# Optimization experiments

Hardware: AMD Instinct MI355X
Metric: run time of the kernel (lower is better)

The kernel has to match this reference:

```python
import jax, jax.numpy as jnp
import numpy as np

N_NODES = 100000
N_EDGES = 1200000
N_FEAT = 128
HIDDEN = 64
N_CLASSES = 40


def setup_inputs() -> dict:
    key = jax.random.key(0)
    k1, k2, k3, k4 = jax.random.split(key, 4)
    x = jax.random.normal(k1, (N_NODES, N_FEAT), dtype=jnp.float32)
    edge_index = jax.random.randint(k2, (2, N_EDGES), 0, N_NODES, dtype=jnp.int64)
    # Glorot-style init for the linear weights (as in PyG GCNConv)
    W1 = jax.random.normal(k3, (N_FEAT, HIDDEN), dtype=jnp.float32) * (1.0 / np.sqrt(N_FEAT))
    b1 = jnp.zeros((HIDDEN,), dtype=jnp.float32)
    W2 = jax.random.normal(k4, (HIDDEN, N_CLASSES), dtype=jnp.float32) * (1.0 / np.sqrt(HIDDEN))
    b2 = jnp.zeros((N_CLASSES,), dtype=jnp.float32)
    return {"x": x, "edge_index": edge_index, "W1": W1, "b1": b1, "W2": W2, "b2": b2}


def _gcn_conv(x, row, col, dinv, W, b):
    # x: [N, Fin], W: [Fin, Fout]. Transform then normalized scatter-add aggregation.
    h = x @ W                                  # [N, Fout]
    norm = dinv[row] * dinv[col]               # [E'] symmetric normalization
    msgs = h[row] * norm[:, None]              # [E', Fout] gather + scale
    out = jax.ops.segment_sum(msgs, col, num_segments=x.shape[0])  # scatter-add
    return out + b


def reference(x, edge_index, W1, b1, W2, b2):
    N = x.shape[0]
    loops = jnp.arange(N, dtype=edge_index.dtype)
    # add self loops (PyG GCNConv default)
    row = jnp.concatenate([edge_index[0], loops])
    col = jnp.concatenate([edge_index[1], loops])
    deg = jax.ops.segment_sum(jnp.ones_like(col, dtype=x.dtype), col, num_segments=N)
    dinv = jax.lax.rsqrt(deg)  # deg >= 1 thanks to self loops
    h = jax.nn.relu(_gcn_conv(x, row, col, dinv, W1, b1))
    # dropout is identity at inference (training=False)
    return _gcn_conv(h, row, col, dinv, W2, b2)
```

## Files before the change

### kernel.cpp

```cpp
#include <hip/hip_runtime.h>
#include <hip/hip_fp16.h>
#include <type_traits>

#define N_NODES 100000
#define N_EDGES 1200000
#define N_FEAT 128
#define HIDDEN 64
#define N_CLASSES 40

#define BSHIFT 9
#define BMASK 511
#define BUCKET_NODES 512
#define NBK ((N_NODES + BUCKET_NODES - 1) / BUCKET_NODES)
#define BCAP 8192
#define CHUNK 2048

typedef _Float16 f16x8 __attribute__((ext_vector_type(8)));
typedef float f32x4 __attribute__((ext_vector_type(4)));


__global__ __launch_bounds__(256) void bucket_kernel(const int* __restrict__ row,
                                                     const int* __restrict__ col,
                                                     int* __restrict__ gcursor,
                                                     unsigned* __restrict__ bke, int E) {
    __shared__ int hist[NBK];
    __shared__ int pfx[NBK];
    __shared__ int gbase[NBK];
    __shared__ int lcnt[NBK];
    __shared__ unsigned ord[CHUNK];
    __shared__ unsigned char obkt[CHUNK];

    const int t = threadIdx.x;
    const int e0 = blockIdx.x * CHUNK;
    const int nE = min(CHUNK, E - e0);

    for (int i = t; i < NBK; i += 256) {
        hist[i] = 0;
        lcnt[i] = 0;
    }
    __syncthreads();

    for (int i = t; i < nE; i += 256) atomicAdd(&hist[col[e0 + i] >> BSHIFT], 1);
    __syncthreads();

    int v = (t < NBK) ? hist[t] : 0;
    if (t < NBK) pfx[t] = v;
    __syncthreads();
    for (int d = 1; d < 256; d <<= 1) {
        int add = (t >= d && t < NBK) ? pfx[t - d] : 0;
        __syncthreads();
        if (t < NBK) pfx[t] += add;
        __syncthreads();
    }
    if (t < NBK) {
        pfx[t] -= v;
        gbase[t] = t * BCAP + ((v > 0) ? atomicAdd(&gcursor[t], v) : 0);
    }
    __syncthreads();

    for (int i = t; i < nE; i += 256) {
        int r = row[e0 + i];
        int c = col[e0 + i];
        int b = c >> BSHIFT;
        int pos = pfx[b] + atomicAdd(&lcnt[b], 1);
        ord[pos] = ((unsigned)r << BSHIFT) | (unsigned)(c & BMASK);
        obkt[pos] = (unsigned char)b;
    }
    __syncthreads();

    for (int i = t; i < nE; i += 256) {
        int b = obkt[i];
        bke[(size_t)gbase[b] + (i - pfx[b])] = ord[i];
    }
}


__global__ __launch_bounds__(256) void place_kernel(const int* __restrict__ gcursor,
                                                    const unsigned* __restrict__ bke,
                                                    int* __restrict__ rowptr,
                                                    float* __restrict__ dinv,
                                                    int* __restrict__ csr_src, int n) {
    __shared__ int hist[BUCKET_NODES];
    __shared__ int cur[BUCKET_NODES];
    __shared__ int tsum[256];

    const int b = blockIdx.x, t = threadIdx.x;
    const int node0 = b << BSHIFT;
    const int nNodes = min(BUCKET_NODES, n - node0);

    const int myCnt = (t < NBK) ? gcursor[t] : 0;
    tsum[t] = myCnt;
    __syncthreads();
    for (int d = 1; d < 256; d <<= 1) {
        int add = (t >= d) ? tsum[t - d] : 0;
        __syncthreads();
        tsum[t] += add;
        __syncthreads();
    }
    const int base = tsum[b] - gcursor[b];
    const int nb = gcursor[b];
    __syncthreads();

    hist[t] = 0;
    hist[t + 256] = 0;
    __syncthreads();

    const unsigned* src = bke + (size_t)b * BCAP;
    for (int i = t; i < nb; i += 256) atomicAdd(&hist[src[i] & BMASK], 1);
    __syncthreads();

    const int c0 = hist[2 * t];
    const int c1 = hist[2 * t + 1];
    const int s = c0 + c1;
    tsum[t] = s;
    __syncthreads();
    for (int d = 1; d < 256; d <<= 1) {
        int add = (t >= d) ? tsum[t - d] : 0;
        __syncthreads();
        tsum[t] += add;
        __syncthreads();
    }
    const int e0 = base + tsum[t] - s;
    const int e1 = e0 + c0;

    cur[2 * t] = e0;
    cur[2 * t + 1] = e1;
    if (2 * t < nNodes) {
        rowptr[node0 + 2 * t] = e0;
        dinv[node0 + 2 * t] = rsqrtf((float)(c0 + 1));
    }
    if (2 * t + 1 < nNodes) {
        rowptr[node0 + 2 * t + 1] = e1;
        dinv[node0 + 2 * t + 1] = rsqrtf((float)(c1 + 1));
    }
    if (t == 0 && node0 + nNodes == n) rowptr[n] = N_EDGES;
    __syncthreads();

    for (int i = t; i < nb; i += 256) {
        unsigned p = src[i];
        int pos = atomicAdd(&cur[p & BMASK], 1);
        csr_src[pos] = (int)(p >> BSHIFT);
    }
}


template <typename XT, int K, int XSTRIDE, int NOUT, int NOUT_PAD, int OSTRIDE>
__global__ __launch_bounds__(256) void gemm_mfma_kernel(const XT* __restrict__ X,
                                                        const float* __restrict__ W,
                                                        const float* __restrict__ dinv,
                                                        __half* __restrict__ Hs, int M) {
    constexpr int KCH = K / 32;
    constexpr int NT = NOUT_PAD / 16;
    constexpr int WPITCH = NOUT_PAD + 2;

    __shared__ _Float16 wh[K * WPITCH];
    __shared__ float sdinv[256];

    const int tid = threadIdx.x;
    const int bnode0 = blockIdx.x * 256;

    for (int i = tid; i < K * NOUT_PAD; i += 256) {
        int k = i / NOUT_PAD, n = i % NOUT_PAD;
        wh[k * WPITCH + n] = (n < NOUT) ? (_Float16)W[k * NOUT + n] : (_Float16)0.0f;
    }
    {
        int node = bnode0 + tid;
        sdinv[tid] = (node < M) ? dinv[node] : 0.f;
    }
    __syncthreads();

    const int wid = tid >> 6;
    const int lane = tid & 63;
    const int m = lane & 15;
    const int quad = lane >> 4;

    f16x8 bf[KCH][NT];
#pragma unroll
    for (int kc = 0; kc < KCH; ++kc)
#pragma unroll
        for (int nt = 0; nt < NT; ++nt)
#pragma unroll
            for (int j = 0; j < 8; ++j)
                bf[kc][nt][j] = wh[(kc * 32 + quad * 8 + j) * WPITCH + nt * 16 + m];

    for (int nt4 = 0; nt4 < 4; ++nt4) {
        const int nb = bnode0 + wid * 64 + nt4 * 16;
        if (nb >= M) break;
        const int rowi = min(nb + m, M - 1);
        const XT* xr = X + (size_t)rowi * XSTRIDE;

        f32x4 acc[NT];
#pragma unroll
        for (int nt = 0; nt < NT; ++nt) acc[nt] = (f32x4){0.f, 0.f, 0.f, 0.f};

#pragma unroll
        for (int kc = 0; kc < KCH; ++kc) {
            f16x8 af;
            if constexpr (std::is_same<XT, float>::value) {
                float4 u0 = *(const float4*)&xr[kc * 32 + quad * 8];
                float4 u1 = *(const float4*)&xr[kc * 32 + quad * 8 + 4];
                af[0] = (_Float16)u0.x;
                af[1] = (_Float16)u0.y;
                af[2] = (_Float16)u0.z;
                af[3] = (_Float16)u0.w;
                af[4] = (_Float16)u1.x;
                af[5] = (_Float16)u1.y;
                af[6] = (_Float16)u1.z;
                af[7] = (_Float16)u1.w;
            } else {
                af = *(const f16x8*)&xr[kc * 32 + quad * 8];
            }
#pragma unroll
            for (int nt = 0; nt < NT; ++nt)
                acc[nt] = __builtin_amdgcn_mfma_f32_16x16x32_f16(af, bf[kc][nt], acc[nt], 0, 0, 0);
        }

#pragma unroll
        for (int reg = 0; reg < 4; ++reg) {
            const int node = nb + quad * 4 + reg;
            if (node < M) {
                const float s = sdinv[node - bnode0];
#pragma unroll
                for (int nt = 0; nt < NT; ++nt) {
                    const int f = nt * 16 + m;
                    if (NOUT == NOUT_PAD || f < NOUT)
                        Hs[(size_t)node * OSTRIDE + f] = __float2half(acc[nt][reg] * s);
                }
            }
        }
    }
}


__device__ inline void acc_row8(float (&acc)[8], uint4 u) {
    const __half2* hp = (const __half2*)&u;
#pragma unroll
    for (int k = 0; k < 4; ++k) {
        float2 f = __half22float2(hp[k]);
        acc[2 * k] += f.x;
        acc[2 * k + 1] += f.y;
    }
}

template <typename OutT, int FCHUNKS, int HSTRIDE, int OUTSTRIDE, bool RELU>
__global__ __launch_bounds__(256) void gather8_kernel(const int* __restrict__ rowptr,
                                                      const int* __restrict__ csr_src,
                                                      const float* __restrict__ dinv,
                                                      const __half* __restrict__ hs,
                                                      const float* __restrict__ b,
                                                      OutT* __restrict__ out, int n) {
    const int wave = (blockIdx.x * blockDim.x + threadIdx.x) >> 6;
    const int lane = threadIdx.x & 63;
    if (wave >= n) return;
    const int c = wave;
    const int g = lane >> 3;
    const int q = lane & 7;
    const bool qv = q < FCHUNKS;

    const float dc = dinv[c];
    const int eBeg = rowptr[c];
    const int eEnd = rowptr[c + 1];

    float acc[8];
#pragma unroll
    for (int j = 0; j < 8; ++j) acc[j] = 0.f;

    if (g == 0 && qv) {
        uint4 u = *(const uint4*)&hs[(size_t)c * HSTRIDE + q * 8];
        acc_row8(acc, u);
    }

    for (int e = eBeg; e < eEnd; e += 16) {
        const int i0 = e + g;
        const int i1 = e + 8 + g;
        int r0 = (i0 < eEnd) ? csr_src[i0] : -1;
        int r1 = (i1 < eEnd) ? csr_src[i1] : -1;
        uint4 u0 = make_uint4(0, 0, 0, 0);
        uint4 u1 = make_uint4(0, 0, 0, 0);
        if (r0 >= 0 && qv) u0 = *(const uint4*)&hs[(size_t)r0 * HSTRIDE + q * 8];
        if (r1 >= 0 && qv) u1 = *(const uint4*)&hs[(size_t)r1 * HSTRIDE + q * 8];
        acc_row8(acc, u0);
        acc_row8(acc, u1);
    }

#pragma unroll
    for (int m = 8; m <= 32; m <<= 1)
#pragma unroll
        for (int j = 0; j < 8; ++j) acc[j] += __shfl_xor(acc[j], m, 64);

    if (g == 0 && qv) {
        float o[8];
#pragma unroll
        for (int j = 0; j < 8; ++j) {
            float v = fmaf(acc[j], dc, b[q * 8 + j]);
            o[j] = RELU ? fmaxf(v, 0.f) : v;
        }
        if constexpr (std::is_same<OutT, float>::value) {
            float* dst = &out[(size_t)c * OUTSTRIDE + q * 8];
            *(float4*)dst = make_float4(o[0], o[1], o[2], o[3]);
            *(float4*)(dst + 4) = make_float4(o[4], o[5], o[6], o[7]);
        } else {
            __half2 pk[4];
#pragma unroll
            for (int k = 0; k < 4; ++k) pk[k] = __floats2half2_rn(o[2 * k], o[2 * k + 1]);
            *(uint4*)&out[(size_t)c * OUTSTRIDE + q * 8] = *(uint4*)pk;
        }
    }
}


extern "C" void kernel_launch(void* const* d_in, const int* in_sizes, int n_in,
                              void* d_out, int out_size, void* d_ws, size_t ws_size,
                              hipStream_t stream) {
    const float* x = (const float*)d_in[0];
    const int* row = (const int*)d_in[1];
    const int* col = row + N_EDGES;
    const float* W1 = (const float*)d_in[2];
    const float* b1 = (const float*)d_in[3];
    const float* W2 = (const float*)d_in[4];
    const float* b2 = (const float*)d_in[5];
    float* out = (float*)d_out;

    const int N = N_NODES, E = N_EDGES;

    char* p = (char*)d_ws;
    auto alloc = [&](size_t bytes) {
        char* q = p;
        p += (bytes + 255) & ~(size_t)255;
        return q;
    };
    int* rowptr = (int*)alloc((size_t)(N + 1) * 4);
    int* csr_src = (int*)alloc((size_t)E * 4);
    int* gcursor = (int*)alloc((size_t)NBK * 4);
    unsigned* bke = (unsigned*)alloc((size_t)NBK * BCAP * 4);
    float* dinv = (float*)alloc((size_t)N * 4);
    __half* h1s = (__half*)alloc((size_t)N * HIDDEN * 2);
    __half* agg1h = (__half*)alloc((size_t)N * HIDDEN * 2);
    __half* h2s = (__half*)alloc((size_t)N * N_CLASSES * 2);

    hipMemsetAsync(gcursor, 0, (size_t)NBK * 4, stream);
    bucket_kernel<<<(E + CHUNK - 1) / CHUNK, 256, 0, stream>>>(row, col, gcursor, bke, E);
    place_kernel<<<NBK, 256, 0, stream>>>(gcursor, bke, rowptr, dinv, csr_src, N);

    gemm_mfma_kernel<float, N_FEAT, N_FEAT, HIDDEN, HIDDEN, HIDDEN>
        <<<(N + 255) / 256, 256, 0, stream>>>(x, W1, dinv, h1s, N);
    gather8_kernel<__half, 8, HIDDEN, HIDDEN, true>
        <<<(N + 3) / 4, 256, 0, stream>>>(rowptr, csr_src, dinv, h1s, b1, agg1h, N);

    gemm_mfma_kernel<_Float16, HIDDEN, HIDDEN, N_CLASSES, 48, N_CLASSES>
        <<<(N + 255) / 256, 256, 0, stream>>>((const _Float16*)agg1h, W2, dinv, h2s, N);
    gather8_kernel<float, 5, N_CLASSES, N_CLASSES, false>
        <<<(N + 3) / 4, 256, 0, stream>>>(rowptr, csr_src, dinv, h2s, b2, out, N);
}
```

Baseline: 235.4 us.

## Map eight nodes per wave in gather and use fma_mix for fp16 accumulation

New measurement: 215.9 us. 1.09x faster.

```diff
diff --git a/kernel.cpp b/kernel.cpp
--- a/kernel.cpp
+++ b/kernel.cpp
@@ -232,32 +232,34 @@
 }
 
 
-__device__ inline void acc_row8(float (&acc)[8], uint4 u) {
-    const __half2* hp = (const __half2*)&u;
+__device__ inline void acc_mix16(float (&acc)[8], uint4 u, float one) {
+    const unsigned* w = (const unsigned*)&u;
 #pragma unroll
     for (int k = 0; k < 4; ++k) {
-        float2 f = __half22float2(hp[k]);
-        acc[2 * k] += f.x;
-        acc[2 * k + 1] += f.y;
+        asm("v_fma_mix_f32 %0, %1, %2, %0 op_sel:[0,0,0] op_sel_hi:[1,0,0]"
+            : "+v"(acc[2 * k])
+            : "v"(w[k]), "v"(one));
+        asm("v_fma_mix_f32 %0, %1, %2, %0 op_sel:[1,0,0] op_sel_hi:[1,0,0]"
+            : "+v"(acc[2 * k + 1])
+            : "v"(w[k]), "v"(one));
     }
 }
 
 template <typename OutT, int FCHUNKS, int HSTRIDE, int OUTSTRIDE, bool RELU>
-__global__ __launch_bounds__(256) void gather8_kernel(const int* __restrict__ rowptr,
-                                                      const int* __restrict__ csr_src,
-                                                      const float* __restrict__ dinv,
-                                                      const __half* __restrict__ hs,
-                                                      const float* __restrict__ b,
-                                                      OutT* __restrict__ out, int n) {
+__global__ __launch_bounds__(256) void gather_g8_kernel(const int* __restrict__ rowptr,
+                                                        const int* __restrict__ csr_src,
+                                                        const float* __restrict__ dinv,
+                                                        const __half* __restrict__ hs,
+                                                        const float* __restrict__ bias,
+                                                        OutT* __restrict__ out, int n) {
     const int wave = (blockIdx.x * blockDim.x + threadIdx.x) >> 6;
     const int lane = threadIdx.x & 63;
-    if (wave >= n) return;
-    const int c = wave;
     const int g = lane >> 3;
     const int q = lane & 7;
-    const bool qv = q < FCHUNKS;
-
-    const float dc = dinv[c];
+    const int c = wave * 8 + g;
+    if (c >= n || q >= FCHUNKS) return;
+
+    const float one = 1.0f;
     const int eBeg = rowptr[c];
     const int eEnd = rowptr[c + 1];
 
@@ -265,46 +267,41 @@
 #pragma unroll
     for (int j = 0; j < 8; ++j) acc[j] = 0.f;
 
-    if (g == 0 && qv) {
-        uint4 u = *(const uint4*)&hs[(size_t)c * HSTRIDE + q * 8];
-        acc_row8(acc, u);
-    }
-
-    for (int e = eBeg; e < eEnd; e += 16) {
-        const int i0 = e + g;
-        const int i1 = e + 8 + g;
-        int r0 = (i0 < eEnd) ? csr_src[i0] : -1;
-        int r1 = (i1 < eEnd) ? csr_src[i1] : -1;
-        uint4 u0 = make_uint4(0, 0, 0, 0);
-        uint4 u1 = make_uint4(0, 0, 0, 0);
-        if (r0 >= 0 && qv) u0 = *(const uint4*)&hs[(size_t)r0 * HSTRIDE + q * 8];
-        if (r1 >= 0 && qv) u1 = *(const uint4*)&hs[(size_t)r1 * HSTRIDE + q * 8];
-        acc_row8(acc, u0);
-        acc_row8(acc, u1);
-    }
-
-#pragma unroll
-    for (int m = 8; m <= 32; m <<= 1)
-#pragma unroll
-        for (int j = 0; j < 8; ++j) acc[j] += __shfl_xor(acc[j], m, 64);
-
-    if (g == 0 && qv) {
-        float o[8];
-#pragma unroll
-        for (int j = 0; j < 8; ++j) {
-            float v = fmaf(acc[j], dc, b[q * 8 + j]);
-            o[j] = RELU ? fmaxf(v, 0.f) : v;
-        }
-        if constexpr (std::is_same<OutT, float>::value) {
-            float* dst = &out[(size_t)c * OUTSTRIDE + q * 8];
-            *(float4*)dst = make_float4(o[0], o[1], o[2], o[3]);
-            *(float4*)(dst + 4) = make_float4(o[4], o[5], o[6], o[7]);
-        } else {
-            __half2 pk[4];
-#pragma unroll
-            for (int k = 0; k < 4; ++k) pk[k] = __floats2half2_rn(o[2 * k], o[2 * k + 1]);
-            *(uint4*)&out[(size_t)c * OUTSTRIDE + q * 8] = *(uint4*)pk;
-        }
+    const __half* hq = hs + q * 8;
+
+    acc_mix16(acc, *(const uint4*)(hq + (size_t)c * HSTRIDE), one);
+
+    int e = eBeg;
+    for (; e + 2 <= eEnd; e += 2) {
+        int r0 = csr_src[e];
+        int r1 = csr_src[e + 1];
+        uint4 u0 = *(const uint4*)(hq + (size_t)r0 * HSTRIDE);
+        uint4 u1 = *(const uint4*)(hq + (size_t)r1 * HSTRIDE);
+        acc_mix16(acc, u0, one);
+        acc_mix16(acc, u1, one);
+    }
+    if (e < eEnd) {
+        int r = csr_src[e];
+        acc_mix16(acc, *(const uint4*)(hq + (size_t)r * HSTRIDE), one);
+    }
+
+    const float dc = dinv[c];
+    float o[8];
+#pragma unroll
+    for (int j = 0; j < 8; ++j) {
+        float v = fmaf(acc[j], dc, bias[q * 8 + j]);
+        o[j] = RELU ? fmaxf(v, 0.f) : v;
+    }
+
+    if constexpr (std::is_same<OutT, float>::value) {
+        float* dst = &out[(size_t)c * OUTSTRIDE + q * 8];
+        *(float4*)dst = make_float4(o[0], o[1], o[2], o[3]);
+        *(float4*)(dst + 4) = make_float4(o[4], o[5], o[6], o[7]);
+    } else {
+        __half2 pk[4];
+#pragma unroll
+        for (int k = 0; k < 4; ++k) pk[k] = __floats2half2_rn(o[2 * k], o[2 * k + 1]);
+        *(uint4*)&out[(size_t)c * OUTSTRIDE + q * 8] = *(uint4*)pk;
     }
 }
 
@@ -344,11 +341,11 @@
 
     gemm_mfma_kernel<float, N_FEAT, N_FEAT, HIDDEN, HIDDEN, HIDDEN>
         <<<(N + 255) / 256, 256, 0, stream>>>(x, W1, dinv, h1s, N);
-    gather8_kernel<__half, 8, HIDDEN, HIDDEN, true>
-        <<<(N + 3) / 4, 256, 0, stream>>>(rowptr, csr_src, dinv, h1s, b1, agg1h, N);
+    gather_g8_kernel<__half, 8, HIDDEN, HIDDEN, true>
+        <<<(N + 31) / 32, 256, 0, stream>>>(rowptr, csr_src, dinv, h1s, b1, agg1h, N);
 
     gemm_mfma_kernel<_Float16, HIDDEN, HIDDEN, N_CLASSES, 48, N_CLASSES>
         <<<(N + 255) / 256, 256, 0, stream>>>((const _Float16*)agg1h, W2, dinv, h2s, N);
-    gather8_kernel<float, 5, N_CLASSES, N_CLASSES, false>
-        <<<(N + 3) / 4, 256, 0, stream>>>(rowptr, csr_src, dinv, h2s, b2, out, N);
-}
+    gather_g8_kernel<float, 5, N_CLASSES, N_CLASSES, false>
+        <<<(N + 31) / 32, 256, 0, stream>>>(rowptr, csr_src, dinv, h2s, b2, out, N);
+}
```
